# Optimization experiments

Hardware: AMD Instinct MI355X
Metric: run time of the kernel (lower is better)

Reference implementation:

```python
import jax, jax.numpy as jnp
import numpy as np

S = 5            # num_species
B = 1_000_000    # batch (proteins)
D = 32           # input_dim == hidden_dim (hard-coded 32 in forward)
EPS = 1e-5       # torch BatchNorm1d default eps
BRANCH_WEIGHT = 0.92


def setup_inputs() -> dict:
    key = jax.random.key(0)
    ks = jax.random.split(key, 20)
    f32 = jnp.float32
    inp = {
        "network_feat": jax.random.normal(ks[0], (B, D), f32),
        "species_ids": jax.random.randint(ks[1], (B,), 0, S),
        # per-species params, stacked along species axis. Weights stored [in, out]
        # (transpose of torch nn.Linear layout) so y = x @ W + b.
        "W1": jax.random.normal(ks[2], (S, D, D), f32) * 0.1,
        "b1": jax.random.normal(ks[3], (S, D), f32) * 0.1,
        "bn1_gamma": jax.random.uniform(ks[4], (S, D), f32, 0.5, 1.5),
        "bn1_beta": jax.random.normal(ks[5], (S, D), f32) * 0.1,
        "bn1_mean": jax.random.normal(ks[6], (S, D), f32) * 0.1,
        "bn1_var": jax.random.uniform(ks[7], (S, D), f32, 0.5, 1.5),
        "W2": jax.random.normal(ks[8], (S, D, D), f32) * 0.1,
        "b2": jax.random.normal(ks[9], (S, D), f32) * 0.1,
        "bn2_gamma": jax.random.uniform(ks[10], (S, D), f32, 0.5, 1.5),
        "bn2_beta": jax.random.normal(ks[11], (S, D), f32) * 0.1,
        "bn2_mean": jax.random.normal(ks[12], (S, D), f32) * 0.1,
        "bn2_var": jax.random.uniform(ks[13], (S, D), f32, 0.5, 1.5),
        "Wsc": jax.random.normal(ks[14], (S, D, D), f32) * 0.1,
        "bsc": jax.random.normal(ks[15], (S, D), f32) * 0.1,
        "Wsh": jax.random.normal(ks[16], (D, D), f32) * 0.1,
        "bsh": jax.random.normal(ks[17], (D,), f32) * 0.1,
    }
    return inp


def _bn(h, gamma, beta, mean, var):
    # BatchNorm1d in eval mode: running-stat normalization + affine.
    return (h - mean) * jax.lax.rsqrt(var + EPS) * gamma + beta


def reference(network_feat, species_ids, W1, b1, bn1_gamma, bn1_beta, bn1_mean,
              bn1_var, W2, b2, bn2_gamma, bn2_beta, bn2_mean, bn2_var,
              Wsc, bsc, Wsh, bsh):
    # Eval mode: dropout = identity, BN uses running stats.
    # Instead of gather/scatter per species, compute each species' tiny MLP on the
    # full batch and select with the species mask (same math; dense & fusible).
    x = network_feat
    out = jnp.zeros_like(x)
    for s in range(S):  # small fixed expert count
        shortcut = x @ Wsc[s] + bsc[s]
        h = jax.nn.relu(x @ W1[s] + b1[s])
        h = _bn(h, bn1_gamma[s], bn1_beta[s], bn1_mean[s], bn1_var[s])
        h = jax.nn.relu(h @ W2[s] + b2[s] + shortcut)
        h = _bn(h, bn2_gamma[s], bn2_beta[s], bn2_mean[s], bn2_var[s])
        mask = (species_ids == s)[:, None]  # [B, 1]
        out = jnp.where(mask, h, out)
    out = jax.nn.relu(out @ Wsh + bsh)  # shared MLP (dropout inactive)
    return out * BRANCH_WEIGHT
```

## Files before the change

kernel.cpp:

```cpp
#include <hip/hip_runtime.h>


#define EPSBN 1e-5f
#define TPB 256
#define NBLKMAX 1024
#define WIN 256

typedef __attribute__((ext_vector_type(8))) short bf16x8;
typedef __attribute__((ext_vector_type(16))) float f32x16;
typedef __attribute__((ext_vector_type(4))) unsigned u32x4;

union FU { unsigned u[4]; bf16x8 v; u32x4 q; };

static __device__ __forceinline__ unsigned pkbf(float lo, float hi) {
    unsigned r;
    asm("v_cvt_pk_bf16_f32 %0, %1, %2" : "=v"(r) : "v"(lo), "v"(hi));
    return r;
}

__global__ void k_pre(unsigned* __restrict__ wfrag, float* __restrict__ bconst,
                      const float* __restrict__ W1, const float* __restrict__ b1,
                      const float* __restrict__ g1, const float* __restrict__ be1,
                      const float* __restrict__ mu1, const float* __restrict__ va1,
                      const float* __restrict__ W2, const float* __restrict__ b2,
                      const float* __restrict__ g2, const float* __restrict__ be2,
                      const float* __restrict__ mu2, const float* __restrict__ va2,
                      const float* __restrict__ Wsc, const float* __restrict__ bsc,
                      const float* __restrict__ Wsh, const float* __restrict__ bsh) {
    if (blockIdx.x < 40) {
        const int i = blockIdx.x * 256 + threadIdx.x;
        const int p = i & 3, l = (i >> 2) & 63, c = (i >> 8) & 1;
        const int m = (i >> 9) & 3, s = i >> 11;
        const int ln = l & 31, hi = l >> 5;
        const int k0 = c * 16 + hi * 8 + 2 * p;
        float lo, hv;
        if (m == 0)      { lo = W1[s*1024 + k0*32 + ln];  hv = W1[s*1024 + (k0+1)*32 + ln]; }
        else if (m == 1) { lo = Wsc[s*1024 + k0*32 + ln]; hv = Wsc[s*1024 + (k0+1)*32 + ln]; }
        else if (m == 2) {
            float A0 = g1[s*32+k0]   * rsqrtf(va1[s*32+k0]   + EPSBN);
            float A1 = g1[s*32+k0+1] * rsqrtf(va1[s*32+k0+1] + EPSBN);
            lo = A0 * W2[s*1024 + k0*32 + ln]; hv = A1 * W2[s*1024 + (k0+1)*32 + ln];
        } else {
            float A0 = 0.92f * g2[s*32+k0]   * rsqrtf(va2[s*32+k0]   + EPSBN);
            float A1 = 0.92f * g2[s*32+k0+1] * rsqrtf(va2[s*32+k0+1] + EPSBN);
            lo = A0 * Wsh[k0*32 + ln]; hv = A1 * Wsh[(k0+1)*32 + ln];
        }
        wfrag[i] = pkbf(lo, hv);
    } else {
        for (int i = threadIdx.x; i < 480; i += 256) {
            const int reg = i & 15, hi = (i >> 4) & 1, t = i >> 5;
            const int q = t % 3, s = t / 3;
            const int r = (reg & 3) + 8 * (reg >> 2) + 4 * hi;
            float v;
            if (q == 0) v = b1[s*32 + r];
            else if (q == 1) {
                v = b2[s*32 + r] + bsc[s*32 + r];
                for (int k = 0; k < 32; ++k) {
                    float A = g1[s*32+k] * rsqrtf(va1[s*32+k] + EPSBN);
                    float C = be1[s*32+k] - mu1[s*32+k] * A;
                    v = fmaf(C, W2[s*1024 + k*32 + r], v);
                }
            } else {
                v = bsh[r];
                for (int k = 0; k < 32; ++k) {
                    float A = g2[s*32+k] * rsqrtf(va2[s*32+k] + EPSBN);
                    float C = be2[s*32+k] - mu2[s*32+k] * A;
                    v = fmaf(C, Wsh[k*32 + r], v);
                }
                v *= 0.92f;
            }
            bconst[i] = v;
        }
    }
}

static __device__ __forceinline__ void reluT(const f32x16& c, bf16x8& f0, bf16x8& f1) {
    unsigned p[8];
    #pragma unroll
    for (int i = 0; i < 8; ++i)
        p[i] = pkbf(fmaxf(c[2 * i], 0.f), fmaxf(c[2 * i + 1], 0.f));
    auto s0 = __builtin_amdgcn_permlane32_swap(p[0], p[2], false, false);
    auto s1 = __builtin_amdgcn_permlane32_swap(p[1], p[3], false, false);
    auto s2 = __builtin_amdgcn_permlane32_swap(p[4], p[6], false, false);
    auto s3 = __builtin_amdgcn_permlane32_swap(p[5], p[7], false, false);
    FU u0, u1;
    u0.u[0] = s0[0]; u0.u[1] = s1[0]; u0.u[2] = s0[1]; u0.u[3] = s1[1];
    u1.u[0] = s2[0]; u1.u[1] = s3[0]; u1.u[2] = s2[1]; u1.u[3] = s3[1];
    f0 = u0.v; f1 = u1.v;
}

static __device__ __forceinline__ void store_row(float* __restrict__ op, const f32x16& a3) {
    #pragma unroll
    for (int q = 0; q < 4; ++q) {
        float4 v;
        v.x = fmaxf(a3[4 * q + 0], 0.f);
        v.y = fmaxf(a3[4 * q + 1], 0.f);
        v.z = fmaxf(a3[4 * q + 2], 0.f);
        v.w = fmaxf(a3[4 * q + 3], 0.f);
        *(float4*)(op + q * 8) = v;
    }
}

__global__ __launch_bounds__(TPB, 4) void k_main(
    const float* __restrict__ X, const int* __restrict__ sid,
    const unsigned* __restrict__ wfrag, const float* __restrict__ bconst,
    float* __restrict__ out, int B) {
    __shared__ __align__(16) unsigned char xb[16384];
    __shared__ float clds[480];
    __shared__ int idxl[416];
    __shared__ int wq[4][5];
    __shared__ int tspec[16];
    __shared__ int sgb[8];

    const int tid = threadIdx.x;
    const int l   = tid & 63;
    const int ln  = l & 31;
    const int hi  = l >> 5;
    const int wav = tid >> 6;
    const unsigned long long ltmask = (1ull << l) - 1ull;

    for (int i = tid; i < 480; i += TPB) clds[i] = bconst[i];

    const int nwin = (B + WIN - 1) / WIN;
    for (int w = blockIdx.x; w < nwin; w += gridDim.x) {
        __syncthreads();
        const int wbase = w * WIN;

        const long fmax = (long)B * 32 - 8;
        #pragma unroll
        for (int k = 0; k < 4; ++k) {
            long fo = (long)wbase * 32 + k * 2048 + tid * 8;
            if (fo > fmax) fo = fmax;
            float4 xa = *(const float4*)(X + fo);
            float4 xc = *(const float4*)(X + fo + 4);
            FU u;
            u.u[0] = pkbf(xa.x, xa.y); u.u[1] = pkbf(xa.z, xa.w);
            u.u[2] = pkbf(xc.x, xc.y); u.u[3] = pkbf(xc.z, xc.w);
            const int row  = k * 64 + (tid >> 2);
            const int slot = (tid & 3) ^ (row & 3);
            *(u32x4*)(xb + row * 64 + slot * 16) = u.q;
        }

        const int myrow = wbase + tid;
        const int s = (myrow < B) ? sid[myrow] : -1;
        int prank = 0;
        #pragma unroll
        for (int sp = 0; sp < 5; ++sp) {
            unsigned long long m = __ballot(s == sp);
            if (l == 0) wq[wav][sp] = (int)__popcll(m);
            if (s == sp) prank = (int)__popcll(m & ltmask);
        }
        for (int i = tid; i < 416; i += TPB) idxl[i] = -1;
        __syncthreads();

        if (tid == 0) {
            int o = 0, tt = 0;
            for (int sp = 0; sp < 5; ++sp) {
                int c = wq[0][sp] + wq[1][sp] + wq[2][sp] + wq[3][sp];
                sgb[sp] = o;
                int nt = (c + 31) >> 5;
                for (int kk = 0; kk < nt; ++kk) tspec[tt++] = sp;
                o += nt << 5;
            }
            sgb[5] = tt;
        }
        __syncthreads();

        if (s >= 0) {
            int off = sgb[s] + prank;
            for (int w2 = 0; w2 < wav; ++w2) off += wq[w2][s];
            idxl[off] = tid;
        }
        __syncthreads();

        const int ntl = sgb[5];
        for (int t = wav; t < ntl; t += 4) {
            const int csp = __builtin_amdgcn_readfirstlane(tspec[t]);
            const int lid = idxl[t * 32 + ln];
            const int r = lid < 0 ? 0 : lid;

            const unsigned* wp = wfrag + csp * 2048;
            FU w00, w01, w10, w11, w20, w21, w30, w31;
            w00.q = *(const u32x4*)(wp + (0 * 64 + l) * 4);
            w01.q = *(const u32x4*)(wp + (1 * 64 + l) * 4);
            w10.q = *(const u32x4*)(wp + (2 * 64 + l) * 4);
            w11.q = *(const u32x4*)(wp + (3 * 64 + l) * 4);
            w20.q = *(const u32x4*)(wp + (4 * 64 + l) * 4);
            w21.q = *(const u32x4*)(wp + (5 * 64 + l) * 4);
            w30.q = *(const u32x4*)(wp + (6 * 64 + l) * 4);
            w31.q = *(const u32x4*)(wp + (7 * 64 + l) * 4);

            const float* cp = clds + csp * 96;
            f32x16 a1 = *(const f32x16*)(cp + hi * 16);
            f32x16 a2 = *(const f32x16*)(cp + 32 + hi * 16);

            const int rs = r & 3;
            const bf16x8 b0 = *(const bf16x8*)(xb + r * 64 + ((hi ^ rs) << 4));
            const bf16x8 b1 = *(const bf16x8*)(xb + r * 64 + (((2 + hi) ^ rs) << 4));

            a1 = __builtin_amdgcn_mfma_f32_32x32x16_bf16(w00.v, b0, a1, 0, 0, 0);
            a2 = __builtin_amdgcn_mfma_f32_32x32x16_bf16(w10.v, b0, a2, 0, 0, 0);
            a1 = __builtin_amdgcn_mfma_f32_32x32x16_bf16(w01.v, b1, a1, 0, 0, 0);
            a2 = __builtin_amdgcn_mfma_f32_32x32x16_bf16(w11.v, b1, a2, 0, 0, 0);

            bf16x8 h0, h1;
            reluT(a1, h0, h1);
            a2 = __builtin_amdgcn_mfma_f32_32x32x16_bf16(w20.v, h0, a2, 0, 0, 0);
            a2 = __builtin_amdgcn_mfma_f32_32x32x16_bf16(w21.v, h1, a2, 0, 0, 0);

            bf16x8 g0, g1;
            reluT(a2, g0, g1);
            f32x16 a3 = *(const f32x16*)(cp + 64 + hi * 16);
            a3 = __builtin_amdgcn_mfma_f32_32x32x16_bf16(w30.v, g0, a3, 0, 0, 0);
            a3 = __builtin_amdgcn_mfma_f32_32x32x16_bf16(w31.v, g1, a3, 0, 0, 0);

            if (lid >= 0) store_row(out + (long)(wbase + lid) * 32 + hi * 4, a3);
        }
    }
}

extern "C" void kernel_launch(void* const* d_in, const int* in_sizes, int n_in,
                              void* d_out, int out_size, void* d_ws, size_t ws_size,
                              hipStream_t stream) {
    const float* X   = (const float*)d_in[0];
    const int*   sid = (const int*)d_in[1];
    const float* W1  = (const float*)d_in[2];
    const float* b1  = (const float*)d_in[3];
    const float* g1  = (const float*)d_in[4];
    const float* be1 = (const float*)d_in[5];
    const float* mu1 = (const float*)d_in[6];
    const float* va1 = (const float*)d_in[7];
    const float* W2  = (const float*)d_in[8];
    const float* b2  = (const float*)d_in[9];
    const float* g2  = (const float*)d_in[10];
    const float* be2 = (const float*)d_in[11];
    const float* mu2 = (const float*)d_in[12];
    const float* va2 = (const float*)d_in[13];
    const float* Wsc = (const float*)d_in[14];
    const float* bsc = (const float*)d_in[15];
    const float* Wsh = (const float*)d_in[16];
    const float* bsh = (const float*)d_in[17];
    float* out = (float*)d_out;
    const int B = in_sizes[1];

    unsigned* wfrag = (unsigned*)d_ws;
    float* bconst   = (float*)(wfrag + 10240);

    k_pre<<<41, 256, 0, stream>>>(wfrag, bconst,
                                  W1, b1, g1, be1, mu1, va1,
                                  W2, b2, g2, be2, mu2, va2,
                                  Wsc, bsc, Wsh, bsh);

    const int nwin = (B + WIN - 1) / WIN;
    const int nblocks = min(NBLKMAX, nwin);
    k_main<<<nblocks, TPB, 0, stream>>>(X, sid, wfrag, bconst, out, B);
}
```

Before: 71.41 us.

## Use one 512-row window per block and prefetch next tile's weight fragments

Replaces the persistent grid-stride loop (up to 1024 blocks over 256-row windows) with one block per 512-row window, launching about 1954 blocks. Each thread now computes the per-species tile boundaries itself, which removes the single-thread scan and two barriers. The next tile's species weights are loaded while the current tile's MFMAs run. Doubling the LDS staging buffer to 32KB may lower occupancy, and the non-persistent grid gives up reuse of the loaded constants across windows.

```diff
diff --git a/kernel.cpp b/kernel.cpp
--- a/kernel.cpp
+++ b/kernel.cpp
@@ -3,8 +3,7 @@
 
 #define EPSBN 1e-5f
 #define TPB 256
-#define NBLKMAX 1024
-#define WIN 256
+#define WIN 512
 
 typedef __attribute__((ext_vector_type(8))) short bf16x8;
 typedef __attribute__((ext_vector_type(16))) float f32x16;
@@ -105,12 +104,10 @@
     const float* __restrict__ X, const int* __restrict__ sid,
     const unsigned* __restrict__ wfrag, const float* __restrict__ bconst,
     float* __restrict__ out, int B) {
-    __shared__ __align__(16) unsigned char xb[16384];
+    __shared__ __align__(16) unsigned char xb[32768];
     __shared__ float clds[480];
-    __shared__ int idxl[416];
-    __shared__ int wq[4][5];
-    __shared__ int tspec[16];
-    __shared__ int sgb[8];
+    __shared__ int idxl[672];
+    __shared__ int wq[2][4][5];
 
     const int tid = threadIdx.x;
     const int l   = tid & 63;
@@ -118,69 +115,126 @@
     const int hi  = l >> 5;
     const int wav = tid >> 6;
     const unsigned long long ltmask = (1ull << l) - 1ull;
+    const int wbase = blockIdx.x * WIN;
 
     for (int i = tid; i < 480; i += TPB) clds[i] = bconst[i];
 
-    const int nwin = (B + WIN - 1) / WIN;
-    for (int w = blockIdx.x; w < nwin; w += gridDim.x) {
-        __syncthreads();
-        const int wbase = w * WIN;
-
-        const long fmax = (long)B * 32 - 8;
-        #pragma unroll
-        for (int k = 0; k < 4; ++k) {
-            long fo = (long)wbase * 32 + k * 2048 + tid * 8;
-            if (fo > fmax) fo = fmax;
-            float4 xa = *(const float4*)(X + fo);
-            float4 xc = *(const float4*)(X + fo + 4);
-            FU u;
-            u.u[0] = pkbf(xa.x, xa.y); u.u[1] = pkbf(xa.z, xa.w);
-            u.u[2] = pkbf(xc.x, xc.y); u.u[3] = pkbf(xc.z, xc.w);
-            const int row  = k * 64 + (tid >> 2);
-            const int slot = (tid & 3) ^ (row & 3);
-            *(u32x4*)(xb + row * 64 + slot * 16) = u.q;
-        }
-
-        const int myrow = wbase + tid;
-        const int s = (myrow < B) ? sid[myrow] : -1;
-        int prank = 0;
+    const long fmax = (long)B * 32 - 8;
+    #pragma unroll
+    for (int k = 0; k < 8; ++k) {
+        long fo = (long)wbase * 32 + k * 2048 + tid * 8;
+        if (fo > fmax) fo = fmax;
+        float4 xa = *(const float4*)(X + fo);
+        float4 xc = *(const float4*)(X + fo + 4);
+        FU u;
+        u.u[0] = pkbf(xa.x, xa.y); u.u[1] = pkbf(xa.z, xa.w);
+        u.u[2] = pkbf(xc.x, xc.y); u.u[3] = pkbf(xc.z, xc.w);
+        const int row  = k * 64 + (tid >> 2);
+        const int slot = (tid & 3) ^ (row & 3);
+        *(u32x4*)(xb + row * 64 + slot * 16) = u.q;
+    }
+
+    int sv[2], prank[2];
+    #pragma unroll
+    for (int it = 0; it < 2; ++it) {
+        const int row = wbase + it * TPB + tid;
+        sv[it] = (row < B) ? sid[row] : -1;
+        prank[it] = 0;
         #pragma unroll
         for (int sp = 0; sp < 5; ++sp) {
-            unsigned long long m = __ballot(s == sp);
-            if (l == 0) wq[wav][sp] = (int)__popcll(m);
-            if (s == sp) prank = (int)__popcll(m & ltmask);
-        }
-        for (int i = tid; i < 416; i += TPB) idxl[i] = -1;
-        __syncthreads();
-
-        if (tid == 0) {
-            int o = 0, tt = 0;
-            for (int sp = 0; sp < 5; ++sp) {
-                int c = wq[0][sp] + wq[1][sp] + wq[2][sp] + wq[3][sp];
-                sgb[sp] = o;
-                int nt = (c + 31) >> 5;
-                for (int kk = 0; kk < nt; ++kk) tspec[tt++] = sp;
-                o += nt << 5;
-            }
-            sgb[5] = tt;
-        }
-        __syncthreads();
-
+            unsigned long long m = __ballot(sv[it] == sp);
+            if (l == 0) wq[it][wav][sp] = (int)__popcll(m);
+            if (sv[it] == sp) prank[it] = (int)__popcll(m & ltmask);
+        }
+    }
+    for (int i = tid; i < 672; i += TPB) idxl[i] = -1;
+    __syncthreads();
+
+    int tb[6];
+    {
+        int t = 0;
+        #pragma unroll
+        for (int sp = 0; sp < 5; ++sp) {
+            tb[sp] = t;
+            int c = 0;
+            #pragma unroll
+            for (int it = 0; it < 2; ++it)
+                #pragma unroll
+                for (int w2 = 0; w2 < 4; ++w2) c += wq[it][w2][sp];
+            t += (c + 31) >> 5;
+        }
+        tb[5] = t;
+    }
+
+    #pragma unroll
+    for (int it = 0; it < 2; ++it) {
+        const int s = sv[it];
         if (s >= 0) {
-            int off = sgb[s] + prank;
-            for (int w2 = 0; w2 < wav; ++w2) off += wq[w2][s];
-            idxl[off] = tid;
-        }
-        __syncthreads();
-
-        const int ntl = sgb[5];
-        for (int t = wav; t < ntl; t += 4) {
-            const int csp = __builtin_amdgcn_readfirstlane(tspec[t]);
-            const int lid = idxl[t * 32 + ln];
-            const int r = lid < 0 ? 0 : lid;
-
-            const unsigned* wp = wfrag + csp * 2048;
-            FU w00, w01, w10, w11, w20, w21, w30, w31;
+            int off = tb[s] * 32 + prank[it];
+            for (int t2 = 0; t2 < it; ++t2)
+                #pragma unroll
+                for (int w2 = 0; w2 < 4; ++w2) off += wq[t2][w2][s];
+            for (int w2 = 0; w2 < wav; ++w2) off += wq[it][w2][s];
+            idxl[off] = it * TPB + tid;
+        }
+    }
+
+    const int ntl = tb[5];
+    int t = wav;
+    int csp = 0;
+    FU w00, w01, w10, w11, w20, w21, w30, w31;
+    if (t < ntl) {
+        #pragma unroll
+        for (int k = 1; k < 5; ++k) csp += (t >= tb[k]) ? 1 : 0;
+        csp = __builtin_amdgcn_readfirstlane(csp);
+        const unsigned* wp = wfrag + csp * 2048;
+        w00.q = *(const u32x4*)(wp + (0 * 64 + l) * 4);
+        w01.q = *(const u32x4*)(wp + (1 * 64 + l) * 4);
+        w10.q = *(const u32x4*)(wp + (2 * 64 + l) * 4);
+        w11.q = *(const u32x4*)(wp + (3 * 64 + l) * 4);
+        w20.q = *(const u32x4*)(wp + (4 * 64 + l) * 4);
+        w21.q = *(const u32x4*)(wp + (5 * 64 + l) * 4);
+        w30.q = *(const u32x4*)(wp + (6 * 64 + l) * 4);
+        w31.q = *(const u32x4*)(wp + (7 * 64 + l) * 4);
+    }
+    __syncthreads();
+
+    for (; t < ntl; t += 4) {
+        const int lid = idxl[t * 32 + ln];
+        const int r = lid < 0 ? 0 : lid;
+
+        const float* cp = clds + csp * 96;
+        f32x16 a1 = *(const f32x16*)(cp + hi * 16);
+        f32x16 a2 = *(const f32x16*)(cp + 32 + hi * 16);
+
+        const int rs = r & 3;
+        const bf16x8 b0 = *(const bf16x8*)(xb + r * 64 + ((hi ^ rs) << 4));
+        const bf16x8 b1 = *(const bf16x8*)(xb + r * 64 + (((2 + hi) ^ rs) << 4));
+
+        a1 = __builtin_amdgcn_mfma_f32_32x32x16_bf16(w00.v, b0, a1, 0, 0, 0);
+        a2 = __builtin_amdgcn_mfma_f32_32x32x16_bf16(w10.v, b0, a2, 0, 0, 0);
+        a1 = __builtin_amdgcn_mfma_f32_32x32x16_bf16(w01.v, b1, a1, 0, 0, 0);
+        a2 = __builtin_amdgcn_mfma_f32_32x32x16_bf16(w11.v, b1, a2, 0, 0, 0);
+
+        bf16x8 h0, h1;
+        reluT(a1, h0, h1);
+        a2 = __builtin_amdgcn_mfma_f32_32x32x16_bf16(w20.v, h0, a2, 0, 0, 0);
+        a2 = __builtin_amdgcn_mfma_f32_32x32x16_bf16(w21.v, h1, a2, 0, 0, 0);
+
+        bf16x8 g0, g1;
+        reluT(a2, g0, g1);
+        f32x16 a3 = *(const f32x16*)(cp + 64 + hi * 16);
+        a3 = __builtin_amdgcn_mfma_f32_32x32x16_bf16(w30.v, g0, a3, 0, 0, 0);
+        a3 = __builtin_amdgcn_mfma_f32_32x32x16_bf16(w31.v, g1, a3, 0, 0, 0);
+
+        const int tn = t + 4;
+        if (tn < ntl) {
+            int nsp = 0;
+            #pragma unroll
+            for (int k = 1; k < 5; ++k) nsp += (tn >= tb[k]) ? 1 : 0;
+            nsp = __builtin_amdgcn_readfirstlane(nsp);
+            csp = nsp;
+            const unsigned* wp = wfrag + nsp * 2048;
             w00.q = *(const u32x4*)(wp + (0 * 64 + l) * 4);
             w01.q = *(const u32x4*)(wp + (1 * 64 + l) * 4);
             w10.q = *(const u32x4*)(wp + (2 * 64 + l) * 4);
@@ -189,33 +243,9 @@
             w21.q = *(const u32x4*)(wp + (5 * 64 + l) * 4);
             w30.q = *(const u32x4*)(wp + (6 * 64 + l) * 4);
             w31.q = *(const u32x4*)(wp + (7 * 64 + l) * 4);
-
-            const float* cp = clds + csp * 96;
-            f32x16 a1 = *(const f32x16*)(cp + hi * 16);
-            f32x16 a2 = *(const f32x16*)(cp + 32 + hi * 16);
-
-            const int rs = r & 3;
-            const bf16x8 b0 = *(const bf16x8*)(xb + r * 64 + ((hi ^ rs) << 4));
-            const bf16x8 b1 = *(const bf16x8*)(xb + r * 64 + (((2 + hi) ^ rs) << 4));
-
-            a1 = __builtin_amdgcn_mfma_f32_32x32x16_bf16(w00.v, b0, a1, 0, 0, 0);
-            a2 = __builtin_amdgcn_mfma_f32_32x32x16_bf16(w10.v, b0, a2, 0, 0, 0);
-            a1 = __builtin_amdgcn_mfma_f32_32x32x16_bf16(w01.v, b1, a1, 0, 0, 0);
-            a2 = __builtin_amdgcn_mfma_f32_32x32x16_bf16(w11.v, b1, a2, 0, 0, 0);
-
-            bf16x8 h0, h1;
-            reluT(a1, h0, h1);
-            a2 = __builtin_amdgcn_mfma_f32_32x32x16_bf16(w20.v, h0, a2, 0, 0, 0);
-            a2 = __builtin_amdgcn_mfma_f32_32x32x16_bf16(w21.v, h1, a2, 0, 0, 0);
-
-            bf16x8 g0, g1;
-            reluT(a2, g0, g1);
-            f32x16 a3 = *(const f32x16*)(cp + 64 + hi * 16);
-            a3 = __builtin_amdgcn_mfma_f32_32x32x16_bf16(w30.v, g0, a3, 0, 0, 0);
-            a3 = __builtin_amdgcn_mfma_f32_32x32x16_bf16(w31.v, g1, a3, 0, 0, 0);
-
-            if (lid >= 0) store_row(out + (long)(wbase + lid) * 32 + hi * 4, a3);
-        }
+        }
+
+        if (lid >= 0) store_row(out + (long)(wbase + lid) * 32 + hi * 4, a3);
     }
 }
 
@@ -252,6 +282,5 @@
                                   Wsc, bsc, Wsh, bsh);
 
     const int nwin = (B + WIN - 1) / WIN;
-    const int nblocks = min(NBLKMAX, nwin);
-    k_main<<<nblocks, TPB, 0, stream>>>(X, sid, wfrag, bconst, out, B);
-}
+    k_main<<<nwin, TPB, 0, stream>>>(X, sid, wfrag, bconst, out, B);
+}
```

After: 77.17 us. +8.1%, slower.

## Prefetch next window in registers and stage outputs through LDS for coalesced stores

Applied to the files above, without the earlier changes.

Software-pipelines the persistent window loop by loading the next window's X rows and species ids into registers while the current window is being computed. Output rows are written into a swizzled 32 KB LDS buffer and then stored to global memory as fully coalesced float4 rows, replacing scattered per-row stores. The tile bookkeeping moves from a single-thread LDS pass to per-thread register prefix sums, which removes one barrier, and barriers become explicit lgkmcnt waits. The larger LDS footprint and extra registers reduce occupancy, so launch bounds drop to 3 waves per EU and the grid cap to 768.

```diff
diff --git a/kernel.cpp b/kernel.cpp
--- a/kernel.cpp
+++ b/kernel.cpp
@@ -3,8 +3,8 @@
 
 #define EPSBN 1e-5f
 #define TPB 256
-#define NBLKMAX 1024
 #define WIN 256
+#define NBLKMAX 768
 
 typedef __attribute__((ext_vector_type(8))) short bf16x8;
 typedef __attribute__((ext_vector_type(16))) float f32x16;
@@ -16,6 +16,11 @@
     unsigned r;
     asm("v_cvt_pk_bf16_f32 %0, %1, %2" : "=v"(r) : "v"(lo), "v"(hi));
     return r;
+}
+
+static __device__ __forceinline__ void ldsbar() {
+    asm volatile("s_waitcnt lgkmcnt(0)" ::: "memory");
+    __builtin_amdgcn_s_barrier();
 }
 
 __global__ void k_pre(unsigned* __restrict__ wfrag, float* __restrict__ bconst,
@@ -89,28 +94,15 @@
     f0 = u0.v; f1 = u1.v;
 }
 
-static __device__ __forceinline__ void store_row(float* __restrict__ op, const f32x16& a3) {
-    #pragma unroll
-    for (int q = 0; q < 4; ++q) {
-        float4 v;
-        v.x = fmaxf(a3[4 * q + 0], 0.f);
-        v.y = fmaxf(a3[4 * q + 1], 0.f);
-        v.z = fmaxf(a3[4 * q + 2], 0.f);
-        v.w = fmaxf(a3[4 * q + 3], 0.f);
-        *(float4*)(op + q * 8) = v;
-    }
-}
-
-__global__ __launch_bounds__(TPB, 4) void k_main(
+__global__ __launch_bounds__(TPB, 3) void k_main(
     const float* __restrict__ X, const int* __restrict__ sid,
     const unsigned* __restrict__ wfrag, const float* __restrict__ bconst,
     float* __restrict__ out, int B) {
     __shared__ __align__(16) unsigned char xb[16384];
+    __shared__ __align__(16) float ob[8192];
     __shared__ float clds[480];
     __shared__ int idxl[416];
     __shared__ int wq[4][5];
-    __shared__ int tspec[16];
-    __shared__ int sgb[8];
 
     const int tid = threadIdx.x;
     const int l   = tid & 63;
@@ -122,27 +114,39 @@
     for (int i = tid; i < 480; i += TPB) clds[i] = bconst[i];
 
     const int nwin = (B + WIN - 1) / WIN;
-    for (int w = blockIdx.x; w < nwin; w += gridDim.x) {
-        __syncthreads();
+    const long fmaxo = (long)B * 32 - 8;
+
+    float4 pa[4], pb[4];
+    int svp = -1;
+
+    int w0 = blockIdx.x;
+    if (w0 < nwin) {
+        #pragma unroll
+        for (int k = 0; k < 4; ++k) {
+            long fo = (long)w0 * (WIN * 32) + k * 2048 + tid * 8;
+            if (fo > fmaxo) fo = fmaxo;
+            pa[k] = *(const float4*)(X + fo);
+            pb[k] = *(const float4*)(X + fo + 4);
+        }
+        int row = w0 * WIN + tid;
+        svp = (row < B) ? sid[row < B ? row : B - 1] : -1;
+    }
+
+    for (int w = w0; w < nwin; w += gridDim.x) {
         const int wbase = w * WIN;
-
-        const long fmax = (long)B * 32 - 8;
+        const int rows = min(WIN, B - wbase);
+
         #pragma unroll
         for (int k = 0; k < 4; ++k) {
-            long fo = (long)wbase * 32 + k * 2048 + tid * 8;
-            if (fo > fmax) fo = fmax;
-            float4 xa = *(const float4*)(X + fo);
-            float4 xc = *(const float4*)(X + fo + 4);
             FU u;
-            u.u[0] = pkbf(xa.x, xa.y); u.u[1] = pkbf(xa.z, xa.w);
-            u.u[2] = pkbf(xc.x, xc.y); u.u[3] = pkbf(xc.z, xc.w);
+            u.u[0] = pkbf(pa[k].x, pa[k].y); u.u[1] = pkbf(pa[k].z, pa[k].w);
+            u.u[2] = pkbf(pb[k].x, pb[k].y); u.u[3] = pkbf(pb[k].z, pb[k].w);
             const int row  = k * 64 + (tid >> 2);
             const int slot = (tid & 3) ^ (row & 3);
             *(u32x4*)(xb + row * 64 + slot * 16) = u.q;
         }
 
-        const int myrow = wbase + tid;
-        const int s = (myrow < B) ? sid[myrow] : -1;
+        const int s = svp;
         int prank = 0;
         #pragma unroll
         for (int sp = 0; sp < 5; ++sp) {
@@ -151,31 +155,45 @@
             if (s == sp) prank = (int)__popcll(m & ltmask);
         }
         for (int i = tid; i < 416; i += TPB) idxl[i] = -1;
-        __syncthreads();
-
-        if (tid == 0) {
-            int o = 0, tt = 0;
+        ldsbar();
+
+        int tb[6];
+        {
+            int t = 0;
+            #pragma unroll
             for (int sp = 0; sp < 5; ++sp) {
+                tb[sp] = t;
                 int c = wq[0][sp] + wq[1][sp] + wq[2][sp] + wq[3][sp];
-                sgb[sp] = o;
-                int nt = (c + 31) >> 5;
-                for (int kk = 0; kk < nt; ++kk) tspec[tt++] = sp;
-                o += nt << 5;
-            }
-            sgb[5] = tt;
-        }
-        __syncthreads();
-
+                t += (c + 31) >> 5;
+            }
+            tb[5] = t;
+        }
         if (s >= 0) {
-            int off = sgb[s] + prank;
+            int off = tb[s] * 32 + prank;
             for (int w2 = 0; w2 < wav; ++w2) off += wq[w2][s];
             idxl[off] = tid;
         }
-        __syncthreads();
-
-        const int ntl = sgb[5];
+
+        const int wn = w + gridDim.x;
+        if (wn < nwin) {
+            #pragma unroll
+            for (int k = 0; k < 4; ++k) {
+                long fo = (long)wn * (WIN * 32) + k * 2048 + tid * 8;
+                if (fo > fmaxo) fo = fmaxo;
+                pa[k] = *(const float4*)(X + fo);
+                pb[k] = *(const float4*)(X + fo + 4);
+            }
+            int row = wn * WIN + tid;
+            svp = (row < B) ? sid[row] : -1;
+        }
+        ldsbar();
+
+        const int ntl = tb[5];
         for (int t = wav; t < ntl; t += 4) {
-            const int csp = __builtin_amdgcn_readfirstlane(tspec[t]);
+            int csp = 0;
+            #pragma unroll
+            for (int k = 1; k < 5; ++k) csp += (t >= tb[k]) ? 1 : 0;
+            csp = __builtin_amdgcn_readfirstlane(csp);
             const int lid = idxl[t * 32 + ln];
             const int r = lid < 0 ? 0 : lid;
 
@@ -214,7 +232,30 @@
             a3 = __builtin_amdgcn_mfma_f32_32x32x16_bf16(w30.v, g0, a3, 0, 0, 0);
             a3 = __builtin_amdgcn_mfma_f32_32x32x16_bf16(w31.v, g1, a3, 0, 0, 0);
 
-            if (lid >= 0) store_row(out + (long)(wbase + lid) * 32 + hi * 4, a3);
+            if (lid >= 0) {
+                #pragma unroll
+                for (int q = 0; q < 4; ++q) {
+                    float4 v;
+                    v.x = fmaxf(a3[4 * q + 0], 0.f);
+                    v.y = fmaxf(a3[4 * q + 1], 0.f);
+                    v.z = fmaxf(a3[4 * q + 2], 0.f);
+                    v.w = fmaxf(a3[4 * q + 3], 0.f);
+                    const int fs = (hi * 4 + q * 8) ^ ((lid & 7) << 2);
+                    *(float4*)(ob + lid * 32 + fs) = v;
+                }
+            }
+        }
+        ldsbar();
+
+        #pragma unroll
+        for (int k = 0; k < 8; ++k) {
+            const int p = k * TPB + tid;
+            const int row = p >> 3, sl = p & 7;
+            if (row < rows) {
+                const int fs = (sl * 4) ^ ((row & 7) << 2);
+                float4 v = *(const float4*)(ob + row * 32 + fs);
+                *(float4*)(out + (long)(wbase + row) * 32 + sl * 4) = v;
+            }
         }
     }
 }
```

Result: faster. 63.66 us (-10.9%).
